# Kernel optimization log

Hardware: AMD Instinct MI355X
Metric: run time of the kernel (lower is better)

## Reference

```python
import jax, jax.numpy as jnp
import numpy as np

B, T, W, L, H, TW = 4, 8192, 1024, 1024, 8, 4
D = L // H
A_SCALE = 8.0  # RG-LRU 'c' constant


def setup_inputs() -> dict:
    key = jax.random.key(0)
    ks = jax.random.split(key, 12)
    nrm = lambda k, shape, std: jax.random.normal(k, shape, jnp.float32) * std
    x = jax.random.normal(ks[0], (B, T, W), jnp.float32)
    segment_pos = jnp.tile(jnp.arange(T, dtype=jnp.int32)[None, :], (B, 1))
    Wy = nrm(ks[1], (W, L), (1.0 / W) ** 0.5)
    by = jnp.zeros((L,), jnp.float32)
    Wx = nrm(ks[2], (W, L), (1.0 / W) ** 0.5)
    bx = jnp.zeros((L,), jnp.float32)
    Wout = nrm(ks[3], (L, W), (1.0 / L) ** 0.5)
    bout = jnp.zeros((W,), jnp.float32)
    conv_w = nrm(ks[4], (TW, L), (1.0 / (TW * L)) ** 0.5)
    conv_b = jnp.zeros((L,), jnp.float32)
    # a_param init: radius in [0.9, 0.999], stored pre-softplus (Griffin rnn_param_init)
    u = jax.random.uniform(ks[5], (L,), jnp.float32)
    a_real = 0.5 * jnp.log(u * (0.999 ** 2 - 0.9 ** 2) + 0.9 ** 2 + 1e-8)  # negative
    a_param = jnp.log(jnp.expm1(-a_real))  # softplus(a_param) == -a_real
    igate_w = nrm(ks[6], (H, D, D), (1.0 / D) ** 0.5)
    igate_b = jnp.zeros((H, D), jnp.float32)
    agate_w = nrm(ks[7], (H, D, D), (1.0 / D) ** 0.5)
    agate_b = jnp.zeros((H, D), jnp.float32)
    return dict(x=x, segment_pos=segment_pos, Wy=Wy, by=by, Wx=Wx, bx=bx,
                conv_w=conv_w, conv_b=conv_b, a_param=a_param,
                igate_w=igate_w, igate_b=igate_b, agate_w=agate_w, agate_b=agate_b,
                Wout=Wout, bout=bout)


def _forward(x, segment_pos, Wy, by, Wx, bx, conv_w, conv_b, a_param,
             igate_w, igate_b, agate_w, agate_b, Wout, bout):
    pos = segment_pos  # [B, T]
    # gating branch
    y = jax.nn.gelu(x @ Wy + by, approximate=True)  # [B,T,L]
    # recurrent branch: linear_x -> causal depthwise conv1d -> RG-LRU
    u = x @ Wx + bx  # [B,T,L]
    acc = jnp.zeros_like(u)
    for i in range(TW):  # small fixed temporal width
        shift = TW - 1 - i
        u_sh = jnp.pad(u, ((0, 0), (shift, 0), (0, 0)))[:, :T]
        valid = (pos >= shift)[..., None]  # zero across segment boundaries
        acc = acc + jnp.where(valid, u_sh * conv_w[i], 0.0)
    u = acc + conv_b  # [B,T,L]
    # RG-LRU gates (block-diagonal per head)
    ur = u.reshape(B, T, H, D)
    gate_x = jax.nn.sigmoid(jnp.einsum('bthd,hde->bthe', ur, igate_w) + igate_b).reshape(B, T, L)
    gate_a = jax.nn.sigmoid(jnp.einsum('bthd,hde->bthe', ur, agate_w) + agate_b).reshape(B, T, L)
    log_a = -A_SCALE * gate_a * jax.nn.softplus(a_param)  # [B,T,L]
    a = jnp.exp(log_a)
    multiplier = jnp.sqrt(1.0 - jnp.exp(2.0 * log_a))
    reset = (pos == 0)[..., None]
    normed_x = (u * gate_x) * jnp.where(reset, 1.0, multiplier)
    a_m = jnp.where(reset, 0.0, a)
    # linear recurrence h_t = a_t * h_{t-1} + normed_x_t via associative scan
    def combine(c1, c2):
        a1, b1 = c1
        a2, b2 = c2
        return (a1 * a2, a2 * b1 + b2)
    _, h = jax.lax.associative_scan(combine, (a_m, normed_x), axis=1)
    return (h * y) @ Wout + bout  # [B,T,W]


def reference(x, segment_pos, Wy, by, Wx, bx, conv_w, conv_b, a_param,
              igate_w, igate_b, agate_w, agate_b, Wout, bout):
    return _forward(x, segment_pos, Wy, by, Wx, bx, conv_w, conv_b, a_param,
                    igate_w, igate_b, agate_w, agate_b, Wout, bout)
```

## Files before the change

### kernel.cpp

```cpp
#include <hip/hip_runtime.h>
#include <cstdint>
#include <cstddef>

#define B_ 4
#define T_ 8192
#define W_ 1024
#define L_ 1024
#define H_ 8
#define D_ 128
#define TW_ 4
#define BT_ (B_*T_)
#define CHUNK_ 64
#define NCH_ (T_/CHUNK_)

typedef __bf16 bf16_t;
typedef __bf16 bf16x8 __attribute__((ext_vector_type(8)));
typedef float  f32x4  __attribute__((ext_vector_type(4)));

__device__ __forceinline__ float  bf2f(bf16_t x){ return (float)x; }
__device__ __forceinline__ bf16_t f2bf(float x){ return (bf16_t)x; }

__device__ __forceinline__ float sigmoidf_(float z){ return 1.0f/(1.0f + __expf(-z)); }
__device__ __forceinline__ float gelu_tanh(float z){
  float g = 0.7978845608028654f*(z + 0.044715f*z*z*z);
  float e = __expf(-2.0f*fabsf(g));
  float th = (1.0f - e)/(1.0f + e);
  th = copysignf(th, g);
  return 0.5f*z*(1.0f + th);
}
__device__ __forceinline__ float softplusf_(float x){
  return (x > 15.0f) ? x : __logf(1.0f + __expf(x));
}

__device__ __forceinline__ void stage16(const bf16_t* g, bf16_t* l){
  __builtin_amdgcn_global_load_lds((const __attribute__((address_space(1))) void*)g,
                                   (__attribute__((address_space(3))) void*)l, 16, 0, 0);
}
__device__ __forceinline__ void stage_tile(const bf16_t* __restrict__ gbase, int ldg,
                                           bf16_t* lds, int wave, int lane){
  #pragma unroll
  for (int c2 = 0; c2 < 2; ++c2){
    int chunk = wave*2 + c2;
    int row = chunk*16 + (lane >> 2);
    int col = (lane & 3)*8;
    stage16(gbase + (size_t)row*ldg + col, lds + chunk*512 + lane*8);
  }
}

__global__ void __launch_bounds__(256) cvt_kernel(const float* __restrict__ in,
                                                  bf16_t* __restrict__ out, int n8){
  int g = blockIdx.x*256 + threadIdx.x;
  if (g >= n8) return;
  f32x4 a = *(const f32x4*)(in + (size_t)g*8);
  f32x4 b = *(const f32x4*)(in + (size_t)g*8 + 4);
  bf16x8 o;
  #pragma unroll
  for (int e=0;e<4;e++){ o[e] = f2bf(a[e]); o[4+e] = f2bf(b[e]); }
  *(bf16x8*)(out + (size_t)g*8) = o;
}

__global__ void __launch_bounds__(256) transpose_f2b(const float* __restrict__ in,
                                                     bf16_t* __restrict__ out, int R, int C){
  __shared__ float tile[32][33];
  size_t mb = (size_t)blockIdx.z * R * C;
  int c0 = blockIdx.x*32, r0 = blockIdx.y*32;
  int tx = threadIdx.x, ty = threadIdx.y;
  #pragma unroll
  for (int i = ty; i < 32; i += 8)
    tile[i][tx] = in[mb + (size_t)(r0+i)*C + c0 + tx];
  __syncthreads();
  #pragma unroll
  for (int i = ty; i < 32; i += 8)
    out[mb + (size_t)(c0+i)*R + r0 + tx] = f2bf(tile[tx][i]);
}

template<int ACT>
__global__ void __launch_bounds__(256,2) gemm128(
    const bf16_t* __restrict__ A, const bf16_t* __restrict__ Bt,
    const float* __restrict__ bias, void* __restrict__ outp)
{
  __shared__ __align__(16) bf16_t As[128*32];
  __shared__ __align__(16) bf16_t Bs[128*32];
  __shared__ __align__(16) char scr_[4][1280];
  const int K = 1024;
  int tid = threadIdx.x, wave = tid>>6, lane = tid&63;
  int wm = wave>>1, wn = wave&1, q = lane>>4, ml = lane&15;
  int lin = blockIdx.x;
  int nl = (lin & 7)*256 + (lin >> 3);
  int bm = nl >> 3, j = nl & 7;
  const bf16_t* Bp = Bt + (size_t)j*128*K;
  f32x4 acc[4][4] = {};
  for (int k0 = 0; k0 < K; k0 += 32){
    stage_tile(A + (size_t)bm*128*K + k0, K, As, wave, lane);
    stage_tile(Bp + k0, K, Bs, wave, lane);
    __syncthreads();
    bf16x8 af[4], bv[4];
    #pragma unroll
    for (int i=0;i<4;i++) af[i] = *(const bf16x8*)(As + (wm*64 + i*16 + ml)*32 + q*8);
    #pragma unroll
    for (int i=0;i<4;i++) bv[i] = *(const bf16x8*)(Bs + (wn*64 + i*16 + ml)*32 + q*8);
    #pragma unroll
    for (int i=0;i<4;i++)
      #pragma unroll
      for (int n=0;n<4;n++)
        acc[i][n] = __builtin_amdgcn_mfma_f32_16x16x32_bf16(af[i], bv[n], acc[i][n], 0,0,0);
    __syncthreads();
  }
  float bb[4];
  #pragma unroll
  for (int n=0;n<4;n++) bb[n] = bias[j*128 + wn*64 + n*16 + ml];
  int rrow = lane>>2, cgp = lane&3;
  size_t mbase = (size_t)bm*128 + wm*64;
  if (ACT == 2){
    float* scrf = (float*)scr_[wave];
    #pragma unroll
    for (int i=0;i<4;i++){
      #pragma unroll
      for (int n=0;n<4;n++){
        #pragma unroll
        for (int r=0;r<4;r++) scrf[(q*4+r)*20 + ml] = acc[i][n][r] + bb[n];
        f32x4 ov = *(const f32x4*)(scrf + rrow*20 + cgp*4);
        size_t grow = mbase + i*16 + rrow;
        *(f32x4*)((float*)outp + grow*1024 + j*128 + wn*64 + n*16 + cgp*4) = ov;
      }
    }
  } else {
    bf16_t* scr = (bf16_t*)scr_[wave];
    #pragma unroll
    for (int np=0;np<2;np++){
      #pragma unroll
      for (int i=0;i<4;i++){
        #pragma unroll
        for (int s=0;s<2;s++){
          int n = np*2+s;
          #pragma unroll
          for (int r=0;r<4;r++){
            float v = acc[i][n][r] + bb[n];
            if (ACT==1) v = gelu_tanh(v);
            scr[(q*4+r)*40 + s*16 + ml] = f2bf(v);
          }
        }
        bf16x8 ov = *(const bf16x8*)(scr + rrow*40 + cgp*8);
        size_t grow = mbase + i*16 + rrow;
        *(bf16x8*)((bf16_t*)outp + grow*1024 + j*128 + wn*64 + np*32 + cgp*8) = ov;
      }
    }
  }
}

__global__ void __launch_bounds__(256,2) gate_kernel(
    const bf16_t* __restrict__ U0,
    const bf16_t* __restrict__ igTw, const bf16_t* __restrict__ agTw,
    const float* __restrict__ igb,  const float* __restrict__ agb,
    const float* __restrict__ a_param,
    const float* __restrict__ conv_w, const float* __restrict__ conv_b,
    const int* __restrict__ segpos,
    bf16_t* __restrict__ XN, bf16_t* __restrict__ L2A)
{
  __shared__ __align__(16) bf16_t As[4*128*32];
  __shared__ __align__(16) char scr_[4][2560];
  int tid = threadIdx.x, wave = tid>>6, lane = tid&63;
  int wm = wave>>1, wn = wave&1, q = lane>>4, ml = lane&15;
  int bm = blockIdx.x, h = blockIdx.y;

  {
    int cg = tid & 15, rg = tid >> 4;
    int col = cg*8;
    int kcc = col >> 5, c32 = col & 31;
    const bf16_t* up = U0 + ((size_t)bm*128 + (size_t)rg*8)*L_ + h*128 + col;
    f32x4 wta[4], wtb[4];
    #pragma unroll
    for (int s=0;s<4;s++){
      wta[s] = *(const f32x4*)(conv_w + (size_t)(3-s)*L_ + h*128 + col);
      wtb[s] = *(const f32x4*)(conv_w + (size_t)(3-s)*L_ + h*128 + col + 4);
    }
    f32x4 cba = *(const f32x4*)(conv_b + h*128 + col);
    f32x4 cbb = *(const f32x4*)(conv_b + h*128 + col + 4);
    bool first = (bm & 63) == 0;
    int r0 = rg*8;
    bf16x8 zero8 = {};
    bf16x8 m1 = (!first || r0 >= 1) ? *(const bf16x8*)(up - 1*L_) : zero8;
    bf16x8 m2 = (!first || r0 >= 2) ? *(const bf16x8*)(up - 2*L_) : zero8;
    bf16x8 m3 = (!first || r0 >= 3) ? *(const bf16x8*)(up - 3*L_) : zero8;
    #pragma unroll
    for (int r=0;r<8;r++){
      bf16x8 cur = *(const bf16x8*)(up + (size_t)r*L_);
      bf16x8 ov;
      #pragma unroll
      for (int e=0;e<4;e++){
        float v0 = cba[e] + bf2f(cur[e])*wta[0][e] + bf2f(m1[e])*wta[1][e]
                          + bf2f(m2[e])*wta[2][e] + bf2f(m3[e])*wta[3][e];
        float v1 = cbb[e] + bf2f(cur[4+e])*wtb[0][e] + bf2f(m1[4+e])*wtb[1][e]
                          + bf2f(m2[4+e])*wtb[2][e] + bf2f(m3[4+e])*wtb[3][e];
        ov[e] = f2bf(v0); ov[4+e] = f2bf(v1);
      }
      *(bf16x8*)(As + kcc*4096 + (size_t)(r0+r)*32 + c32) = ov;
      m3 = m2; m2 = m1; m1 = cur;
    }
  }
  __syncthreads();

  const bf16_t* igp = igTw + (size_t)h*D_*D_;
  const bf16_t* agp = agTw + (size_t)h*D_*D_;
  f32x4 ax[4][4] = {}, aa[4][4] = {};
  #pragma unroll
  for (int kc=0; kc<4; ++kc){
    bf16x8 af[4], bx_[4], ba_[4];
    #pragma unroll
    for (int i=0;i<4;i++) af[i]  = *(const bf16x8*)(As + kc*4096 + (wm*64 + i*16 + ml)*32 + q*8);
    #pragma unroll
    for (int n=0;n<4;n++) bx_[n] = *(const bf16x8*)(igp + (size_t)(wn*64 + n*16 + ml)*128 + kc*32 + q*8);
    #pragma unroll
    for (int n=0;n<4;n++) ba_[n] = *(const bf16x8*)(agp + (size_t)(wn*64 + n*16 + ml)*128 + kc*32 + q*8);
    #pragma unroll
    for (int i=0;i<4;i++)
      #pragma unroll
      for (int n=0;n<4;n++){
        ax[i][n] = __builtin_amdgcn_mfma_f32_16x16x32_bf16(af[i], bx_[n], ax[i][n], 0,0,0);
        aa[i][n] = __builtin_amdgcn_mfma_f32_16x16x32_bf16(af[i], ba_[n], aa[i][n], 0,0,0);
      }
  }

  bf16_t* scrx = (bf16_t*)scr_[wave];
  bf16_t* scra = scrx + 640;
  int rrow = lane>>2, cgp = lane&3;
  size_t mbase = (size_t)bm*128 + wm*64;
  #pragma unroll
  for (int np=0;np<2;np++){
    float bbx2[2], bba2[2], spa2[2]; int kc2[2], ci2[2];
    #pragma unroll
    for (int s=0;s<2;s++){
      int e = wn*64 + (np*2+s)*16 + ml;
      int l = h*D_ + e;
      bbx2[s] = igb[l]; bba2[s] = agb[l]; spa2[s] = softplusf_(a_param[l]);
      kc2[s] = e>>5; ci2[s] = e&31;
    }
    #pragma unroll
    for (int i=0;i<4;i++){
      #pragma unroll
      for (int r=0;r<4;r++){
        int rl = wm*64 + i*16 + q*4 + r;
        size_t row = mbase + i*16 + q*4 + r;
        int pos = segpos[row];
        bool reset = (pos == 0);
        #pragma unroll
        for (int s=0;s<2;s++){
          int n = np*2+s;
          float uval = bf2f(As[kc2[s]*4096 + rl*32 + ci2[s]]);
          float gx = sigmoidf_(ax[i][n][r] + bbx2[s]);
          float ga = sigmoidf_(aa[i][n][r] + bba2[s]);
          float l2a = -8.0f * ga * spa2[s] * 1.4426950408889634f;
          float mult = reset ? 1.0f : sqrtf(fmaxf(0.0f, 1.0f - exp2f(2.0f*l2a)));
          scrx[(q*4+r)*40 + s*16 + ml] = f2bf(uval * gx * mult);
          scra[(q*4+r)*40 + s*16 + ml] = f2bf(reset ? -1e30f : l2a);
        }
      }
      bf16x8 xv = *(const bf16x8*)(scrx + rrow*40 + cgp*8);
      bf16x8 av = *(const bf16x8*)(scra + rrow*40 + cgp*8);
      size_t grow = mbase + i*16 + rrow;
      int gcol = h*D_ + wn*64 + np*32 + cgp*8;
      *(bf16x8*)(XN  + grow*1024 + gcol) = xv;
      *(bf16x8*)(L2A + grow*1024 + gcol) = av;
    }
  }
}

__global__ void __launch_bounds__(128) scan1_kernel(const bf16_t* __restrict__ L2A,
    const bf16_t* __restrict__ XN, float* __restrict__ Aarr, float* __restrict__ Barr)
{
  int lg = threadIdx.x;
  int c = blockIdx.y, b = blockIdx.z;
  int l = lg*8;
  size_t base = ((size_t)b*T_ + (size_t)c*CHUNK_)*L_ + l;
  float suml[8] = {}, brun[8] = {};
  #pragma unroll 4
  for (int t = 0; t < CHUNK_; ++t){
    bf16x8 la = *(const bf16x8*)(L2A + base + (size_t)t*L_);
    bf16x8 xv = *(const bf16x8*)(XN  + base + (size_t)t*L_);
    #pragma unroll
    for (int e=0;e<8;e++){
      float lf = bf2f(la[e]);
      suml[e] += lf;
      brun[e] = exp2f(lf)*brun[e] + bf2f(xv[e]);
    }
  }
  size_t ci = ((size_t)b*NCH_ + c)*L_ + l;
  f32x4 a0, a1, b0, b1;
  #pragma unroll
  for (int e=0;e<4;e++){
    a0[e] = exp2f(suml[e]);   a1[e] = exp2f(suml[4+e]);
    b0[e] = brun[e];          b1[e] = brun[4+e];
  }
  *(f32x4*)(Aarr + ci)     = a0;  *(f32x4*)(Aarr + ci + 4) = a1;
  *(f32x4*)(Barr + ci)     = b0;  *(f32x4*)(Barr + ci + 4) = b1;
}

__global__ void __launch_bounds__(256) scan2_kernel(const float* __restrict__ Aarr,
    const float* __restrict__ Barr, float* __restrict__ Carr)
{
  int l4 = threadIdx.x;
  int b = blockIdx.y;
  f32x4 h = {0.f, 0.f, 0.f, 0.f};
  for (int c = 0; c < NCH_; ++c){
    size_t ci = ((size_t)b*NCH_ + c)*L_ + (size_t)l4*4;
    f32x4 a  = *(const f32x4*)(Aarr + ci);
    f32x4 bb = *(const f32x4*)(Barr + ci);
    *(f32x4*)(Carr + ci) = h;
    #pragma unroll
    for (int e=0;e<4;e++) h[e] = a[e]*h[e] + bb[e];
  }
}

__global__ void __launch_bounds__(128) scan3_kernel(const bf16_t* __restrict__ L2A,
    const bf16_t* __restrict__ XN, const bf16_t* __restrict__ Y,
    const float* __restrict__ Carr, bf16_t* __restrict__ HY)
{
  int lg = threadIdx.x;
  int c = blockIdx.y, b = blockIdx.z;
  int l = lg*8;
  size_t base = ((size_t)b*T_ + (size_t)c*CHUNK_)*L_ + l;
  size_t ci = ((size_t)b*NCH_ + c)*L_ + l;
  f32x4 h0 = *(const f32x4*)(Carr + ci);
  f32x4 h1 = *(const f32x4*)(Carr + ci + 4);
  float h[8];
  #pragma unroll
  for (int e=0;e<4;e++){ h[e] = h0[e]; h[4+e] = h1[e]; }
  #pragma unroll 4
  for (int t = 0; t < CHUNK_; ++t){
    bf16x8 la = *(const bf16x8*)(L2A + base + (size_t)t*L_);
    bf16x8 xv = *(const bf16x8*)(XN  + base + (size_t)t*L_);
    bf16x8 yv = *(const bf16x8*)(Y   + base + (size_t)t*L_);
    bf16x8 o;
    #pragma unroll
    for (int e=0;e<8;e++){
      h[e] = exp2f(bf2f(la[e]))*h[e] + bf2f(xv[e]);
      o[e] = f2bf(h[e]*bf2f(yv[e]));
    }
    *(bf16x8*)(HY + base + (size_t)t*L_) = o;
  }
}

extern "C" void kernel_launch(void* const* d_in, const int* in_sizes, int n_in,
                              void* d_out, int out_size, void* d_ws, size_t ws_size,
                              hipStream_t stream)
{
  (void)in_sizes; (void)n_in; (void)out_size;
  const float* x      = (const float*)d_in[0];
  const int*   segpos = (const int*)  d_in[1];
  const float* Wy     = (const float*)d_in[2];
  const float* by     = (const float*)d_in[3];
  const float* Wx     = (const float*)d_in[4];
  const float* bx     = (const float*)d_in[5];
  const float* conv_w = (const float*)d_in[6];
  const float* conv_b = (const float*)d_in[7];
  const float* a_par  = (const float*)d_in[8];
  const float* igw    = (const float*)d_in[9];
  const float* igb    = (const float*)d_in[10];
  const float* agw    = (const float*)d_in[11];
  const float* agb    = (const float*)d_in[12];
  const float* Wout   = (const float*)d_in[13];
  const float* bout   = (const float*)d_in[14];
  float* out = (float*)d_out;

  char* ws = (char*)d_ws;
  size_t off = 0;
  auto alloc = [&](size_t bytes)->void*{ void* p = ws + off; off += (bytes + 255) & ~(size_t)255; return p; };
  bf16_t* Xbf  = (bf16_t*)alloc((size_t)BT_*W_*2);
  bf16_t* WyT  = (bf16_t*)alloc((size_t)W_*L_*2);
  bf16_t* WxT  = (bf16_t*)alloc((size_t)W_*L_*2);
  bf16_t* WoT  = (bf16_t*)alloc((size_t)L_*W_*2);
  bf16_t* igTw = (bf16_t*)alloc((size_t)H_*D_*D_*2);
  bf16_t* agTw = (bf16_t*)alloc((size_t)H_*D_*D_*2);
  bf16_t* Y    = (bf16_t*)alloc((size_t)BT_*L_*2);
  bf16_t* U0   = (bf16_t*)alloc((size_t)BT_*L_*2);
  bf16_t* XN   = (bf16_t*)alloc((size_t)BT_*L_*2);
  float*  Aarr = (float*) alloc((size_t)B_*NCH_*L_*4);
  float*  Barr = (float*) alloc((size_t)B_*NCH_*L_*4);
  float*  Carr = (float*) alloc((size_t)B_*NCH_*L_*4);
  if (ws_size < off) return;

  bf16_t* L2A = Xbf;
  bf16_t* HY  = U0;

  cvt_kernel<<<dim3(BT_*W_/8/256), 256, 0, stream>>>(x, Xbf, BT_*W_/8);

  dim3 tb(32, 8);
  transpose_f2b<<<dim3(32,32,1), tb, 0, stream>>>(Wy,   WyT, 1024, 1024);
  transpose_f2b<<<dim3(32,32,1), tb, 0, stream>>>(Wx,   WxT, 1024, 1024);
  transpose_f2b<<<dim3(32,32,1), tb, 0, stream>>>(Wout, WoT, 1024, 1024);
  transpose_f2b<<<dim3(4,4,H_),  tb, 0, stream>>>(igw,  igTw, 128, 128);
  transpose_f2b<<<dim3(4,4,H_),  tb, 0, stream>>>(agw,  agTw, 128, 128);

  gemm128<1><<<dim3(2048), 256, 0, stream>>>(Xbf, WyT, by, (void*)Y);
  gemm128<0><<<dim3(2048), 256, 0, stream>>>(Xbf, WxT, bx, (void*)U0);
  gate_kernel<<<dim3(BT_/128, H_), 256, 0, stream>>>(U0, igTw, agTw, igb, agb, a_par,
                                                     conv_w, conv_b, segpos, XN, L2A);
  scan1_kernel<<<dim3(1, NCH_, B_), 128, 0, stream>>>(L2A, XN, Aarr, Barr);
  scan2_kernel<<<dim3(1, B_), 256, 0, stream>>>(Aarr, Barr, Carr);
  scan3_kernel<<<dim3(1, NCH_, B_), 128, 0, stream>>>(L2A, XN, Y, Carr, HY);
  gemm128<2><<<dim3(2048), 256, 0, stream>>>(HY, WoT, bout, (void*)out);
}
```

Measured before the change: 747.2 us.

## Fuse Wy/Wx GEMMs sharing X tile, use fast intrinsics, halve scan chunk

The two input projection GEMMs are merged into one kernel that stages each X tile once and accumulates both Wy and Wx products, so X is read from memory once instead of twice. Transcendentals in GELU, sigmoid, softplus and the scan kernels now use raw amdgcn exp2/rcp/sqrt/log builtins. The scan chunk size drops from 64 to 32, giving more parallel blocks in scan1/scan3 but a longer serial scan2. The fused GEMM doubles its accumulator registers, which may reduce occupancy or cause spills under the launch bound of 2 blocks per CU.

```diff
diff --git a/kernel.cpp b/kernel.cpp
--- a/kernel.cpp
+++ b/kernel.cpp
@@ -10,7 +10,7 @@
 #define D_ 128
 #define TW_ 4
 #define BT_ (B_*T_)
-#define CHUNK_ 64
+#define CHUNK_ 32
 #define NCH_ (T_/CHUNK_)
 
 typedef __bf16 bf16_t;
@@ -20,16 +20,24 @@
 __device__ __forceinline__ float  bf2f(bf16_t x){ return (float)x; }
 __device__ __forceinline__ bf16_t f2bf(float x){ return (bf16_t)x; }
 
-__device__ __forceinline__ float sigmoidf_(float z){ return 1.0f/(1.0f + __expf(-z)); }
-__device__ __forceinline__ float gelu_tanh(float z){
+__device__ __forceinline__ float rcp_ (float x){ return __builtin_amdgcn_rcpf(x); }
+__device__ __forceinline__ float sqrt_(float x){ return __builtin_amdgcn_sqrtf(x); }
+__device__ __forceinline__ float exp2_(float x){ return __builtin_amdgcn_exp2f(x); }
+__device__ __forceinline__ float log2_(float x){ return __builtin_amdgcn_logf(x); }
+#define LOG2E_ 1.4426950408889634f
+
+__device__ __forceinline__ float sigmoid_fast(float z){
+  return rcp_(1.0f + exp2_(-LOG2E_*z));
+}
+__device__ __forceinline__ float softplus_fast(float x){
+  return (x > 15.0f) ? x : 0.6931471805599453f * log2_(1.0f + exp2_(LOG2E_*x));
+}
+__device__ __forceinline__ float gelu_fast(float z){
   float g = 0.7978845608028654f*(z + 0.044715f*z*z*z);
-  float e = __expf(-2.0f*fabsf(g));
-  float th = (1.0f - e)/(1.0f + e);
+  float e = exp2_(-2.8853900817779268f*fabsf(g));
+  float th = (1.0f - e)*rcp_(1.0f + e);
   th = copysignf(th, g);
   return 0.5f*z*(1.0f + th);
-}
-__device__ __forceinline__ float softplusf_(float x){
-  return (x > 15.0f) ? x : __logf(1.0f + __expf(x));
 }
 
 __device__ __forceinline__ void stage16(const bf16_t* g, bf16_t* l){
@@ -74,76 +82,85 @@
     out[mb + (size_t)(c0+i)*R + r0 + tx] = f2bf(tile[tx][i]);
 }
 
-template<int ACT>
-__global__ void __launch_bounds__(256,2) gemm128(
-    const bf16_t* __restrict__ A, const bf16_t* __restrict__ Bt,
-    const float* __restrict__ bias, void* __restrict__ outp)
-{
-  __shared__ __align__(16) bf16_t As[128*32];
-  __shared__ __align__(16) bf16_t Bs[128*32];
-  __shared__ __align__(16) char scr_[4][1280];
-  const int K = 1024;
+__global__ void __launch_bounds__(256,2) gemm_xw_kernel(
+    const bf16_t* __restrict__ X,
+    const bf16_t* __restrict__ WyT, const bf16_t* __restrict__ WxT,
+    const float* __restrict__ by,  const float* __restrict__ bx,
+    bf16_t* __restrict__ Y, bf16_t* __restrict__ U0)
+{
+  __shared__ __align__(16) bf16_t As [128*32];
+  __shared__ __align__(16) bf16_t Bys[128*32];
+  __shared__ __align__(16) bf16_t Bxs[128*32];
+  __shared__ __align__(16) bf16_t scr_g[4][1280];
+  const int K = W_;
   int tid = threadIdx.x, wave = tid>>6, lane = tid&63;
   int wm = wave>>1, wn = wave&1, q = lane>>4, ml = lane&15;
   int lin = blockIdx.x;
   int nl = (lin & 7)*256 + (lin >> 3);
   int bm = nl >> 3, j = nl & 7;
-  const bf16_t* Bp = Bt + (size_t)j*128*K;
-  f32x4 acc[4][4] = {};
+  const bf16_t* Wyp = WyT + (size_t)j*128*K;
+  const bf16_t* Wxp = WxT + (size_t)j*128*K;
+  f32x4 accY[4][4] = {}, accX[4][4] = {};
   for (int k0 = 0; k0 < K; k0 += 32){
-    stage_tile(A + (size_t)bm*128*K + k0, K, As, wave, lane);
-    stage_tile(Bp + k0, K, Bs, wave, lane);
+    stage_tile(X + (size_t)bm*128*K + k0, K, As, wave, lane);
+    stage_tile(Wyp + k0, K, Bys, wave, lane);
+    stage_tile(Wxp + k0, K, Bxs, wave, lane);
     __syncthreads();
-    bf16x8 af[4], bv[4];
-    #pragma unroll
-    for (int i=0;i<4;i++) af[i] = *(const bf16x8*)(As + (wm*64 + i*16 + ml)*32 + q*8);
-    #pragma unroll
-    for (int i=0;i<4;i++) bv[i] = *(const bf16x8*)(Bs + (wn*64 + i*16 + ml)*32 + q*8);
+    bf16x8 af[4], bvy[4], bvx[4];
+    #pragma unroll
+    for (int i=0;i<4;i++) af[i]  = *(const bf16x8*)(As  + (wm*64 + i*16 + ml)*32 + q*8);
+    #pragma unroll
+    for (int i=0;i<4;i++) bvy[i] = *(const bf16x8*)(Bys + (wn*64 + i*16 + ml)*32 + q*8);
+    #pragma unroll
+    for (int i=0;i<4;i++) bvx[i] = *(const bf16x8*)(Bxs + (wn*64 + i*16 + ml)*32 + q*8);
     #pragma unroll
     for (int i=0;i<4;i++)
       #pragma unroll
-      for (int n=0;n<4;n++)
-        acc[i][n] = __builtin_amdgcn_mfma_f32_16x16x32_bf16(af[i], bv[n], acc[i][n], 0,0,0);
+      for (int n=0;n<4;n++){
+        accY[i][n] = __builtin_amdgcn_mfma_f32_16x16x32_bf16(af[i], bvy[n], accY[i][n], 0,0,0);
+        accX[i][n] = __builtin_amdgcn_mfma_f32_16x16x32_bf16(af[i], bvx[n], accX[i][n], 0,0,0);
+      }
     __syncthreads();
   }
-  float bb[4];
-  #pragma unroll
-  for (int n=0;n<4;n++) bb[n] = bias[j*128 + wn*64 + n*16 + ml];
+  float bbY[4], bbX[4];
+  #pragma unroll
+  for (int n=0;n<4;n++){
+    int col = j*128 + wn*64 + n*16 + ml;
+    bbY[n] = by[col]; bbX[n] = bx[col];
+  }
+  bf16_t* s0 = scr_g[wave];
+  bf16_t* s1 = s0 + 640;
   int rrow = lane>>2, cgp = lane&3;
   size_t mbase = (size_t)bm*128 + wm*64;
-  if (ACT == 2){
-    float* scrf = (float*)scr_[wave];
-    #pragma unroll
-    for (int i=0;i<4;i++){
-      #pragma unroll
-      for (int n=0;n<4;n++){
-        #pragma unroll
-        for (int r=0;r<4;r++) scrf[(q*4+r)*20 + ml] = acc[i][n][r] + bb[n];
-        f32x4 ov = *(const f32x4*)(scrf + rrow*20 + cgp*4);
-        size_t grow = mbase + i*16 + rrow;
-        *(f32x4*)((float*)outp + grow*1024 + j*128 + wn*64 + n*16 + cgp*4) = ov;
-      }
-    }
-  } else {
-    bf16_t* scr = (bf16_t*)scr_[wave];
-    #pragma unroll
-    for (int np=0;np<2;np++){
-      #pragma unroll
-      for (int i=0;i<4;i++){
-        #pragma unroll
-        for (int s=0;s<2;s++){
-          int n = np*2+s;
-          #pragma unroll
-          for (int r=0;r<4;r++){
-            float v = acc[i][n][r] + bb[n];
-            if (ACT==1) v = gelu_tanh(v);
-            scr[(q*4+r)*40 + s*16 + ml] = f2bf(v);
-          }
-        }
-        bf16x8 ov = *(const bf16x8*)(scr + rrow*40 + cgp*8);
-        size_t grow = mbase + i*16 + rrow;
-        *(bf16x8*)((bf16_t*)outp + grow*1024 + j*128 + wn*64 + np*32 + cgp*8) = ov;
-      }
+  #pragma unroll
+  for (int i=0;i<4;i++){
+    size_t grow = mbase + i*16 + rrow;
+    int gc = j*128 + wn*64 + cgp*8;
+    #pragma unroll
+    for (int n=0;n<4;n++){
+      bf16_t* sp = (n<2) ? s0 : s1;
+      #pragma unroll
+      for (int r=0;r<4;r++)
+        sp[(q*4+r)*40 + (n&1)*16 + ml] = f2bf(gelu_fast(accY[i][n][r] + bbY[n]));
+    }
+    {
+      bf16x8 v0 = *(const bf16x8*)(s0 + rrow*40 + cgp*8);
+      bf16x8 v1 = *(const bf16x8*)(s1 + rrow*40 + cgp*8);
+      *(bf16x8*)(Y + grow*L_ + gc)      = v0;
+      *(bf16x8*)(Y + grow*L_ + gc + 32) = v1;
+    }
+    #pragma unroll
+    for (int n=0;n<4;n++){
+      bf16_t* sp = (n<2) ? s0 : s1;
+      #pragma unroll
+      for (int r=0;r<4;r++)
+        sp[(q*4+r)*40 + (n&1)*16 + ml] = f2bf(accX[i][n][r] + bbX[n]);
+    }
+    {
+      bf16x8 v0 = *(const bf16x8*)(s0 + rrow*40 + cgp*8);
+      bf16x8 v1 = *(const bf16x8*)(s1 + rrow*40 + cgp*8);
+      *(bf16x8*)(U0 + grow*L_ + gc)      = v0;
+      *(bf16x8*)(U0 + grow*L_ + gc + 32) = v1;
     }
   }
 }
@@ -158,7 +175,7 @@
     bf16_t* __restrict__ XN, bf16_t* __restrict__ L2A)
 {
   __shared__ __align__(16) bf16_t As[4*128*32];
-  __shared__ __align__(16) char scr_[4][2560];
+  __shared__ __align__(16) bf16_t scr_g[4][2560];
   int tid = threadIdx.x, wave = tid>>6, lane = tid&63;
   int wm = wave>>1, wn = wave&1, q = lane>>4, ml = lane&15;
   int bm = blockIdx.x, h = blockIdx.y;
@@ -221,47 +238,51 @@
       }
   }
 
-  bf16_t* scrx = (bf16_t*)scr_[wave];
-  bf16_t* scra = scrx + 640;
+  bf16_t* sx0 = scr_g[wave];
+  bf16_t* sx1 = sx0 + 640;
+  bf16_t* sa0 = sx0 + 1280;
+  bf16_t* sa1 = sx0 + 1920;
   int rrow = lane>>2, cgp = lane&3;
   size_t mbase = (size_t)bm*128 + wm*64;
-  #pragma unroll
-  for (int np=0;np<2;np++){
-    float bbx2[2], bba2[2], spa2[2]; int kc2[2], ci2[2];
-    #pragma unroll
-    for (int s=0;s<2;s++){
-      int e = wn*64 + (np*2+s)*16 + ml;
-      int l = h*D_ + e;
-      bbx2[s] = igb[l]; bba2[s] = agb[l]; spa2[s] = softplusf_(a_param[l]);
-      kc2[s] = e>>5; ci2[s] = e&31;
-    }
-    #pragma unroll
-    for (int i=0;i<4;i++){
-      #pragma unroll
-      for (int r=0;r<4;r++){
-        int rl = wm*64 + i*16 + q*4 + r;
-        size_t row = mbase + i*16 + q*4 + r;
-        int pos = segpos[row];
-        bool reset = (pos == 0);
-        #pragma unroll
-        for (int s=0;s<2;s++){
-          int n = np*2+s;
-          float uval = bf2f(As[kc2[s]*4096 + rl*32 + ci2[s]]);
-          float gx = sigmoidf_(ax[i][n][r] + bbx2[s]);
-          float ga = sigmoidf_(aa[i][n][r] + bba2[s]);
-          float l2a = -8.0f * ga * spa2[s] * 1.4426950408889634f;
-          float mult = reset ? 1.0f : sqrtf(fmaxf(0.0f, 1.0f - exp2f(2.0f*l2a)));
-          scrx[(q*4+r)*40 + s*16 + ml] = f2bf(uval * gx * mult);
-          scra[(q*4+r)*40 + s*16 + ml] = f2bf(reset ? -1e30f : l2a);
-        }
+  float bb_x[4], bb_a[4], spa4[4]; int kc4[4], ci4[4];
+  #pragma unroll
+  for (int n=0;n<4;n++){
+    int e = wn*64 + n*16 + ml;
+    int l = h*D_ + e;
+    bb_x[n] = igb[l]; bb_a[n] = agb[l]; spa4[n] = softplus_fast(a_param[l]);
+    kc4[n] = e>>5; ci4[n] = e&31;
+  }
+  #pragma unroll
+  for (int i=0;i<4;i++){
+    #pragma unroll
+    for (int r=0;r<4;r++){
+      int rl = wm*64 + i*16 + q*4 + r;
+      size_t row = mbase + i*16 + q*4 + r;
+      bool reset = (segpos[row] == 0);
+      #pragma unroll
+      for (int n=0;n<4;n++){
+        float uval = bf2f(As[kc4[n]*4096 + rl*32 + ci4[n]]);
+        float gx = sigmoid_fast(ax[i][n][r] + bb_x[n]);
+        float ga = sigmoid_fast(aa[i][n][r] + bb_a[n]);
+        float l2a = -11.541560327111707f * ga * spa4[n];
+        float mult = reset ? 1.0f : sqrt_(fmaxf(0.0f, 1.0f - exp2_(2.0f*l2a)));
+        bf16_t xnv = f2bf(uval * gx * mult);
+        bf16_t lav = f2bf(reset ? -1e30f : l2a);
+        int so = (q*4+r)*40 + (n&1)*16 + ml;
+        if (n < 2){ sx0[so] = xnv; sa0[so] = lav; }
+        else      { sx1[so] = xnv; sa1[so] = lav; }
       }
-      bf16x8 xv = *(const bf16x8*)(scrx + rrow*40 + cgp*8);
-      bf16x8 av = *(const bf16x8*)(scra + rrow*40 + cgp*8);
-      size_t grow = mbase + i*16 + rrow;
-      int gcol = h*D_ + wn*64 + np*32 + cgp*8;
-      *(bf16x8*)(XN  + grow*1024 + gcol) = xv;
-      *(bf16x8*)(L2A + grow*1024 + gcol) = av;
-    }
+    }
+    size_t grow = mbase + i*16 + rrow;
+    int gc = h*D_ + wn*64 + cgp*8;
+    bf16x8 xv0 = *(const bf16x8*)(sx0 + rrow*40 + cgp*8);
+    bf16x8 xv1 = *(const bf16x8*)(sx1 + rrow*40 + cgp*8);
+    *(bf16x8*)(XN + grow*L_ + gc)      = xv0;
+    *(bf16x8*)(XN + grow*L_ + gc + 32) = xv1;
+    bf16x8 av0 = *(const bf16x8*)(sa0 + rrow*40 + cgp*8);
+    bf16x8 av1 = *(const bf16x8*)(sa1 + rrow*40 + cgp*8);
+    *(bf16x8*)(L2A + grow*L_ + gc)      = av0;
+    *(bf16x8*)(L2A + grow*L_ + gc + 32) = av1;
   }
 }
 
@@ -281,14 +302,14 @@
     for (int e=0;e<8;e++){
       float lf = bf2f(la[e]);
       suml[e] += lf;
-      brun[e] = exp2f(lf)*brun[e] + bf2f(xv[e]);
+      brun[e] = exp2_(lf)*brun[e] + bf2f(xv[e]);
     }
   }
   size_t ci = ((size_t)b*NCH_ + c)*L_ + l;
   f32x4 a0, a1, b0, b1;
   #pragma unroll
   for (int e=0;e<4;e++){
-    a0[e] = exp2f(suml[e]);   a1[e] = exp2f(suml[4+e]);
+    a0[e] = exp2_(suml[e]);   a1[e] = exp2_(suml[4+e]);
     b0[e] = brun[e];          b1[e] = brun[4+e];
   }
   *(f32x4*)(Aarr + ci)     = a0;  *(f32x4*)(Aarr + ci + 4) = a1;
@@ -333,10 +354,60 @@
     bf16x8 o;
     #pragma unroll
     for (int e=0;e<8;e++){
-      h[e] = exp2f(bf2f(la[e]))*h[e] + bf2f(xv[e]);
+      h[e] = exp2_(bf2f(la[e]))*h[e] + bf2f(xv[e]);
       o[e] = f2bf(h[e]*bf2f(yv[e]));
     }
     *(bf16x8*)(HY + base + (size_t)t*L_) = o;
+  }
+}
+
+__global__ void __launch_bounds__(256,2) gemm_out_kernel(
+    const bf16_t* __restrict__ A_, const bf16_t* __restrict__ WoT,
+    const float* __restrict__ bo, float* __restrict__ Out)
+{
+  __shared__ __align__(16) bf16_t As[128*32];
+  __shared__ __align__(16) bf16_t Bs[128*32];
+  __shared__ __align__(16) char scr_[4][1280];
+  const int K = L_;
+  int tid = threadIdx.x, wave = tid>>6, lane = tid&63;
+  int wm = wave>>1, wn = wave&1, q = lane>>4, ml = lane&15;
+  int lin = blockIdx.x;
+  int nl = (lin & 7)*256 + (lin >> 3);
+  int bm = nl >> 3, j = nl & 7;
+  const bf16_t* Bp = WoT + (size_t)j*128*K;
+  f32x4 acc[4][4] = {};
+  for (int k0 = 0; k0 < K; k0 += 32){
+    stage_tile(A_ + (size_t)bm*128*K + k0, K, As, wave, lane);
+    stage_tile(Bp + k0, K, Bs, wave, lane);
+    __syncthreads();
+    bf16x8 af[4], bv[4];
+    #pragma unroll
+    for (int i=0;i<4;i++) af[i] = *(const bf16x8*)(As + (wm*64 + i*16 + ml)*32 + q*8);
+    #pragma unroll
+    for (int i=0;i<4;i++) bv[i] = *(const bf16x8*)(Bs + (wn*64 + i*16 + ml)*32 + q*8);
+    #pragma unroll
+    for (int i=0;i<4;i++)
+      #pragma unroll
+      for (int n=0;n<4;n++)
+        acc[i][n] = __builtin_amdgcn_mfma_f32_16x16x32_bf16(af[i], bv[n], acc[i][n], 0,0,0);
+    __syncthreads();
+  }
+  float bb[4];
+  #pragma unroll
+  for (int n=0;n<4;n++) bb[n] = bo[j*128 + wn*64 + n*16 + ml];
+  float* scrf = (float*)scr_[wave];
+  int rrow = lane>>2, cgp = lane&3;
+  size_t mbase = (size_t)bm*128 + wm*64;
+  #pragma unroll
+  for (int i=0;i<4;i++){
+    size_t grow = mbase + i*16 + rrow;
+    #pragma unroll
+    for (int n=0;n<4;n++){
+      #pragma unroll
+      for (int r=0;r<4;r++) scrf[(q*4+r)*20 + ml] = acc[i][n][r] + bb[n];
+      f32x4 ov = *(const f32x4*)(scrf + rrow*20 + cgp*4);
+      *(f32x4*)(Out + grow*W_ + j*128 + wn*64 + n*16 + cgp*4) = ov;
+    }
   }
 }
 
@@ -391,12 +462,11 @@
   transpose_f2b<<<dim3(4,4,H_),  tb, 0, stream>>>(igw,  igTw, 128, 128);
   transpose_f2b<<<dim3(4,4,H_),  tb, 0, stream>>>(agw,  agTw, 128, 128);
 
-  gemm128<1><<<dim3(2048), 256, 0, stream>>>(Xbf, WyT, by, (void*)Y);
-  gemm128<0><<<dim3(2048), 256, 0, stream>>>(Xbf, WxT, bx, (void*)U0);
+  gemm_xw_kernel<<<dim3(2048), 256, 0, stream>>>(Xbf, WyT, WxT, by, bx, Y, U0);
   gate_kernel<<<dim3(BT_/128, H_), 256, 0, stream>>>(U0, igTw, agTw, igb, agb, a_par,
                                                      conv_w, conv_b, segpos, XN, L2A);
   scan1_kernel<<<dim3(1, NCH_, B_), 128, 0, stream>>>(L2A, XN, Aarr, Barr);
   scan2_kernel<<<dim3(1, B_), 256, 0, stream>>>(Aarr, Barr, Carr);
   scan3_kernel<<<dim3(1, NCH_, B_), 128, 0, stream>>>(L2A, XN, Y, Carr, HY);
-  gemm128<2><<<dim3(2048), 256, 0, stream>>>(HY, WoT, bout, (void*)out);
-}
+  gemm_out_kernel<<<dim3(2048), 256, 0, stream>>>(HY, WoT, bout, out);
+}
```

Measured after the change: 705.0 us. 5.6% less time.
